# Performance work log

Measured on AMD Instinct MI355X. Metric: run time of the kernel, lower is better.

Reference implementation:

```python
import jax, jax.numpy as jnp
import numpy as np

N, D, T = 8192, 512, 262144
MARGIN = 1.0


def setup_inputs() -> dict:
    key = jax.random.key(0)
    k_emb, k_a, k_p, k_n = jax.random.split(key, 4)
    embeddings = jax.random.normal(k_emb, (N, D), dtype=jnp.float32)
    ind_anch = jax.random.randint(k_a, (T,), 0, N, dtype=jnp.int64 if jax.config.jax_enable_x64 else jnp.int32)
    ind_pos = jax.random.randint(k_p, (T,), 0, N, dtype=ind_anch.dtype)
    ind_neg = jax.random.randint(k_n, (T,), 0, N, dtype=ind_anch.dtype)
    return {"embeddings": embeddings, "ind_anch": ind_anch, "ind_pos": ind_pos, "ind_neg": ind_neg}


def reference(embeddings, ind_anch, ind_pos, ind_neg):
    # cosine distance matrix: 1 - normalized @ normalized.T  -> [N, N]
    emb_norm = embeddings / jnp.linalg.norm(embeddings, axis=1, keepdims=True)
    dist_matrix = 1.0 - jnp.matmul(emb_norm, emb_norm.T)
    dist_pos = dist_matrix[ind_anch, ind_pos]
    dist_neg = dist_matrix[ind_anch, ind_neg]
    loss = jax.nn.relu(dist_pos - dist_neg + MARGIN)
    return loss.mean()
```

## Files before the change

### kernel.cpp

```cpp
#include <hip/hip_runtime.h>

constexpr int N_EMB = 8192;
constexpr int D_EMB = 512;
constexpr int T_TRI = 262144;
#define MARGIN_F 1.0f

constexpr int GRID_TRIP = 8192;
constexpr float QSCALE = 512.0f;
constexpr float INV_QS2 = 1.0f / (QSCALE * QSCALE);

constexpr size_t TAB_BYTES = (size_t)N_EMB * D_EMB;

#if __has_builtin(__builtin_amdgcn_sdot4)
__device__ __forceinline__ int dot4(int a, int b, int c) {
    return __builtin_amdgcn_sdot4(a, b, c, false);
}
#else
__device__ __forceinline__ int dot4(int a, int b, int c) {
    c += ((int)(a << 24) >> 24) * ((int)(b << 24) >> 24);
    c += ((int)(a << 16) >> 24) * ((int)(b << 16) >> 24);
    c += ((int)(a <<  8) >> 24) * ((int)(b <<  8) >> 24);
    c += (a >> 24) * (b >> 24);
    return c;
}
#endif

__global__ __launch_bounds__(256) void prep_kernel(const float* __restrict__ emb,
                                                   unsigned char* __restrict__ tab) {
    const int lane = threadIdx.x & 63;
    const int row  = (blockIdx.x << 2) + (threadIdx.x >> 6);
    const float4* p = (const float4*)(emb + (size_t)row * D_EMB);
    float4 v0 = p[2 * lane];
    float4 v1 = p[2 * lane + 1];
    float s = v0.x * v0.x + v0.y * v0.y + v0.z * v0.z + v0.w * v0.w
            + v1.x * v1.x + v1.y * v1.y + v1.z * v1.z + v1.w * v1.w;
#pragma unroll
    for (int off = 32; off > 0; off >>= 1) s += __shfl_xor(s, off, 64);
    const float scl = rsqrtf(s) * QSCALE;

    float q[8] = {v0.x, v0.y, v0.z, v0.w, v1.x, v1.y, v1.z, v1.w};
    int qi[8];
#pragma unroll
    for (int i = 0; i < 8; ++i) {
        float f = rintf(q[i] * scl);
        f = fmaxf(-127.0f, fminf(127.0f, f));
        qi[i] = (int)f;
    }
    unsigned w0 = (qi[0] & 255) | ((qi[1] & 255) << 8) | ((qi[2] & 255) << 16) | ((unsigned)(qi[3] & 255) << 24);
    unsigned w1 = (qi[4] & 255) | ((qi[5] & 255) << 8) | ((qi[6] & 255) << 16) | ((unsigned)(qi[7] & 255) << 24);
    uint2 o; o.x = w0; o.y = w1;
    *(uint2*)(tab + (size_t)row * D_EMB + 8 * lane) = o;
}

__global__ __launch_bounds__(256) void triplet_kernel(const unsigned char* __restrict__ tab,
                                                      const int* __restrict__ ind_a,
                                                      const int* __restrict__ ind_p,
                                                      const int* __restrict__ ind_n,
                                                      float* __restrict__ part) {
    const int lane   = threadIdx.x & 63;
    const int waveIb = threadIdx.x >> 6;
    const int waveId = (blockIdx.x << 2) + waveIb;
    const int tbase  = waveId << 3;

    const int slot = lane & 7;
    const int arr  = lane >> 3;
    const int* ptr = (arr == 0) ? ind_a : ((arr == 1) ? ind_p : ind_n);
    const int myidx = ptr[tbase + slot];

    const int q   = lane >> 4;
    const int sub = lane & 15;
    const int boff = sub << 4;

    const int ia0 = __shfl(myidx, q, 64);
    const int ip0 = __shfl(myidx, 8 + q, 64);
    const int in0 = __shfl(myidx, 16 + q, 64);
    const int ia1 = __shfl(myidx, 4 + q, 64);
    const int ip1 = __shfl(myidx, 12 + q, 64);
    const int in1 = __shfl(myidx, 20 + q, 64);

    const unsigned char* pa0 = tab + ((size_t)ia0 << 9) + boff;
    const unsigned char* pp0 = tab + ((size_t)ip0 << 9) + boff;
    const unsigned char* pn0 = tab + ((size_t)in0 << 9) + boff;
    const unsigned char* pa1 = tab + ((size_t)ia1 << 9) + boff;
    const unsigned char* pp1 = tab + ((size_t)ip1 << 9) + boff;
    const unsigned char* pn1 = tab + ((size_t)in1 << 9) + boff;

    uint4 a00 = *(const uint4*)pa0,        a01 = *(const uint4*)(pa0 + 256);
    uint4 p00 = *(const uint4*)pp0,        p01 = *(const uint4*)(pp0 + 256);
    uint4 n00 = *(const uint4*)pn0,        n01 = *(const uint4*)(pn0 + 256);
    uint4 a10 = *(const uint4*)pa1,        a11 = *(const uint4*)(pa1 + 256);
    uint4 p10 = *(const uint4*)pp1,        p11 = *(const uint4*)(pp1 + 256);
    uint4 n10 = *(const uint4*)pn1,        n11 = *(const uint4*)(pn1 + 256);

    float local = 0.0f;

    {
        int sp = 0, sn = 0;
        sp = dot4((int)a00.x, (int)p00.x, sp); sp = dot4((int)a00.y, (int)p00.y, sp);
        sp = dot4((int)a00.z, (int)p00.z, sp); sp = dot4((int)a00.w, (int)p00.w, sp);
        sp = dot4((int)a01.x, (int)p01.x, sp); sp = dot4((int)a01.y, (int)p01.y, sp);
        sp = dot4((int)a01.z, (int)p01.z, sp); sp = dot4((int)a01.w, (int)p01.w, sp);
        sn = dot4((int)a00.x, (int)n00.x, sn); sn = dot4((int)a00.y, (int)n00.y, sn);
        sn = dot4((int)a00.z, (int)n00.z, sn); sn = dot4((int)a00.w, (int)n00.w, sn);
        sn = dot4((int)a01.x, (int)n01.x, sn); sn = dot4((int)a01.y, (int)n01.y, sn);
        sn = dot4((int)a01.z, (int)n01.z, sn); sn = dot4((int)a01.w, (int)n01.w, sn);
        int d = sn - sp;
#pragma unroll
        for (int m = 1; m < 16; m <<= 1) d += __shfl_xor(d, m, 64);
        if (sub == 0) local += fmaxf(fmaf((float)d, INV_QS2, MARGIN_F), 0.0f);
    }

    {
        int sp = 0, sn = 0;
        sp = dot4((int)a10.x, (int)p10.x, sp); sp = dot4((int)a10.y, (int)p10.y, sp);
        sp = dot4((int)a10.z, (int)p10.z, sp); sp = dot4((int)a10.w, (int)p10.w, sp);
        sp = dot4((int)a11.x, (int)p11.x, sp); sp = dot4((int)a11.y, (int)p11.y, sp);
        sp = dot4((int)a11.z, (int)p11.z, sp); sp = dot4((int)a11.w, (int)p11.w, sp);
        sn = dot4((int)a10.x, (int)n10.x, sn); sn = dot4((int)a10.y, (int)n10.y, sn);
        sn = dot4((int)a10.z, (int)n10.z, sn); sn = dot4((int)a10.w, (int)n10.w, sn);
        sn = dot4((int)a11.x, (int)n11.x, sn); sn = dot4((int)a11.y, (int)n11.y, sn);
        sn = dot4((int)a11.z, (int)n11.z, sn); sn = dot4((int)a11.w, (int)n11.w, sn);
        int d = sn - sp;
#pragma unroll
        for (int m = 1; m < 16; m <<= 1) d += __shfl_xor(d, m, 64);
        if (sub == 0) local += fmaxf(fmaf((float)d, INV_QS2, MARGIN_F), 0.0f);
    }

    local += __shfl_xor(local, 16, 64);
    local += __shfl_xor(local, 32, 64);

    __shared__ float smem[4];
    if (lane == 0) smem[waveIb] = local;
    __syncthreads();
    if (threadIdx.x == 0) {
        part[blockIdx.x] = smem[0] + smem[1] + smem[2] + smem[3];
    }
}

__global__ __launch_bounds__(256) void reduce_kernel(const float* __restrict__ part,
                                                     float* __restrict__ out) {
    float s = 0.0f;
#pragma unroll
    for (int i = 0; i < GRID_TRIP / 256; ++i) s += part[threadIdx.x + 256 * i];
#pragma unroll
    for (int off = 32; off > 0; off >>= 1) s += __shfl_down(s, off, 64);
    __shared__ float sm[4];
    if ((threadIdx.x & 63) == 0) sm[threadIdx.x >> 6] = s;
    __syncthreads();
    if (threadIdx.x == 0) {
        out[0] = (sm[0] + sm[1] + sm[2] + sm[3]) * (1.0f / (float)T_TRI);
    }
}

extern "C" void kernel_launch(void* const* d_in, const int* in_sizes, int n_in,
                              void* d_out, int out_size, void* d_ws, size_t ws_size,
                              hipStream_t stream) {
    const float* emb   = (const float*)d_in[0];
    const int*   ind_a = (const int*)d_in[1];
    const int*   ind_p = (const int*)d_in[2];
    const int*   ind_n = (const int*)d_in[3];
    float* out = (float*)d_out;

    unsigned char* tab = (unsigned char*)d_ws;
    float* part = (float*)((char*)d_ws + TAB_BYTES);

    prep_kernel<<<N_EMB / 4, 256, 0, stream>>>(emb, tab);
    triplet_kernel<<<GRID_TRIP, 256, 0, stream>>>(tab, ind_a, ind_p, ind_n, part);
    reduce_kernel<<<1, 256, 0, stream>>>(part, out);
}
```

Baseline: 92.15 us.

## Process 32 triplets per wave with register double-buffered row gathers

Each wave now handles 32 triplets instead of 8, and the grid shrinks from 8192 to 2048 blocks. Indices are loaded with coalesced per-array reads, and each iteration prefetches the next group's anchor, positive and negative rows into registers while the current group's dot products run. This amortises per-block launch and index overhead and keeps more gathers in flight per wave. The cost is higher register pressure and fewer waves available to hide latency, which the launch bound of 4 blocks is meant to contain.

After: 89.82 us. 2.5% less time.

```diff
diff --git a/kernel.cpp b/kernel.cpp
--- a/kernel.cpp
+++ b/kernel.cpp
@@ -5,7 +5,7 @@
 constexpr int T_TRI = 262144;
 #define MARGIN_F 1.0f
 
-constexpr int GRID_TRIP = 8192;
+constexpr int GRID_TRIP = 2048;
 constexpr float QSCALE = 512.0f;
 constexpr float INV_QS2 = 1.0f / (QSCALE * QSCALE);
 
@@ -52,78 +52,68 @@
     *(uint2*)(tab + (size_t)row * D_EMB + 8 * lane) = o;
 }
 
-__global__ __launch_bounds__(256) void triplet_kernel(const unsigned char* __restrict__ tab,
-                                                      const int* __restrict__ ind_a,
-                                                      const int* __restrict__ ind_p,
-                                                      const int* __restrict__ ind_n,
-                                                      float* __restrict__ part) {
+__global__ __launch_bounds__(256, 4) void triplet_kernel(const unsigned char* __restrict__ tab,
+                                                         const int* __restrict__ ind_a,
+                                                         const int* __restrict__ ind_p,
+                                                         const int* __restrict__ ind_n,
+                                                         float* __restrict__ part) {
     const int lane   = threadIdx.x & 63;
     const int waveIb = threadIdx.x >> 6;
     const int waveId = (blockIdx.x << 2) + waveIb;
-    const int tbase  = waveId << 3;
+    const int tbase  = waveId << 5;
 
-    const int slot = lane & 7;
-    const int arr  = lane >> 3;
-    const int* ptr = (arr == 0) ? ind_a : ((arr == 1) ? ind_p : ind_n);
-    const int myidx = ptr[tbase + slot];
+    const int l5 = lane & 31;
+    const int idxA = ind_a[tbase + l5];
+    const int idxP = ind_p[tbase + l5];
+    const int idxN = ind_n[tbase + l5];
 
-    const int q   = lane >> 4;
-    const int sub = lane & 15;
+    const int q    = lane >> 4;
+    const int sub  = lane & 15;
     const int boff = sub << 4;
 
-    const int ia0 = __shfl(myidx, q, 64);
-    const int ip0 = __shfl(myidx, 8 + q, 64);
-    const int in0 = __shfl(myidx, 16 + q, 64);
-    const int ia1 = __shfl(myidx, 4 + q, 64);
-    const int ip1 = __shfl(myidx, 12 + q, 64);
-    const int in1 = __shfl(myidx, 20 + q, 64);
-
-    const unsigned char* pa0 = tab + ((size_t)ia0 << 9) + boff;
-    const unsigned char* pp0 = tab + ((size_t)ip0 << 9) + boff;
-    const unsigned char* pn0 = tab + ((size_t)in0 << 9) + boff;
-    const unsigned char* pa1 = tab + ((size_t)ia1 << 9) + boff;
-    const unsigned char* pp1 = tab + ((size_t)ip1 << 9) + boff;
-    const unsigned char* pn1 = tab + ((size_t)in1 << 9) + boff;
-
-    uint4 a00 = *(const uint4*)pa0,        a01 = *(const uint4*)(pa0 + 256);
-    uint4 p00 = *(const uint4*)pp0,        p01 = *(const uint4*)(pp0 + 256);
-    uint4 n00 = *(const uint4*)pn0,        n01 = *(const uint4*)(pn0 + 256);
-    uint4 a10 = *(const uint4*)pa1,        a11 = *(const uint4*)(pa1 + 256);
-    uint4 p10 = *(const uint4*)pp1,        p11 = *(const uint4*)(pp1 + 256);
-    uint4 n10 = *(const uint4*)pn1,        n11 = *(const uint4*)(pn1 + 256);
+    int s0 = q;
+    int ia = __shfl(idxA, s0, 64);
+    int ip = __shfl(idxP, s0, 64);
+    int in_ = __shfl(idxN, s0, 64);
+    const uint4* pa = (const uint4*)(tab + ((size_t)ia << 9) + boff);
+    const uint4* pp = (const uint4*)(tab + ((size_t)ip << 9) + boff);
+    const uint4* pn = (const uint4*)(tab + ((size_t)in_ << 9) + boff);
+    uint4 a0 = pa[0], a1 = pa[16];
+    uint4 p0 = pp[0], p1 = pp[16];
+    uint4 n0 = pn[0], n1 = pn[16];
 
     float local = 0.0f;
+#pragma unroll
+    for (int g = 0; g < 8; ++g) {
+        uint4 ba0, ba1, bp0, bp1, bn0, bn1;
+        if (g < 7) {
+            const int s = 4 * (g + 1) + q;
+            const int ja = __shfl(idxA, s, 64);
+            const int jp = __shfl(idxP, s, 64);
+            const int jn = __shfl(idxN, s, 64);
+            const uint4* qa = (const uint4*)(tab + ((size_t)ja << 9) + boff);
+            const uint4* qp = (const uint4*)(tab + ((size_t)jp << 9) + boff);
+            const uint4* qn = (const uint4*)(tab + ((size_t)jn << 9) + boff);
+            ba0 = qa[0]; ba1 = qa[16];
+            bp0 = qp[0]; bp1 = qp[16];
+            bn0 = qn[0]; bn1 = qn[16];
+        }
 
-    {
         int sp = 0, sn = 0;
-        sp = dot4((int)a00.x, (int)p00.x, sp); sp = dot4((int)a00.y, (int)p00.y, sp);
-        sp = dot4((int)a00.z, (int)p00.z, sp); sp = dot4((int)a00.w, (int)p00.w, sp);
-        sp = dot4((int)a01.x, (int)p01.x, sp); sp = dot4((int)a01.y, (int)p01.y, sp);
-        sp = dot4((int)a01.z, (int)p01.z, sp); sp = dot4((int)a01.w, (int)p01.w, sp);
-        sn = dot4((int)a00.x, (int)n00.x, sn); sn = dot4((int)a00.y, (int)n00.y, sn);
-        sn = dot4((int)a00.z, (int)n00.z, sn); sn = dot4((int)a00.w, (int)n00.w, sn);
-        sn = dot4((int)a01.x, (int)n01.x, sn); sn = dot4((int)a01.y, (int)n01.y, sn);
-        sn = dot4((int)a01.z, (int)n01.z, sn); sn = dot4((int)a01.w, (int)n01.w, sn);
+        sp = dot4((int)a0.x, (int)p0.x, sp); sp = dot4((int)a0.y, (int)p0.y, sp);
+        sp = dot4((int)a0.z, (int)p0.z, sp); sp = dot4((int)a0.w, (int)p0.w, sp);
+        sp = dot4((int)a1.x, (int)p1.x, sp); sp = dot4((int)a1.y, (int)p1.y, sp);
+        sp = dot4((int)a1.z, (int)p1.z, sp); sp = dot4((int)a1.w, (int)p1.w, sp);
+        sn = dot4((int)a0.x, (int)n0.x, sn); sn = dot4((int)a0.y, (int)n0.y, sn);
+        sn = dot4((int)a0.z, (int)n0.z, sn); sn = dot4((int)a0.w, (int)n0.w, sn);
+        sn = dot4((int)a1.x, (int)n1.x, sn); sn = dot4((int)a1.y, (int)n1.y, sn);
+        sn = dot4((int)a1.z, (int)n1.z, sn); sn = dot4((int)a1.w, (int)n1.w, sn);
         int d = sn - sp;
 #pragma unroll
         for (int m = 1; m < 16; m <<= 1) d += __shfl_xor(d, m, 64);
         if (sub == 0) local += fmaxf(fmaf((float)d, INV_QS2, MARGIN_F), 0.0f);
-    }
 
-    {
-        int sp = 0, sn = 0;
-        sp = dot4((int)a10.x, (int)p10.x, sp); sp = dot4((int)a10.y, (int)p10.y, sp);
-        sp = dot4((int)a10.z, (int)p10.z, sp); sp = dot4((int)a10.w, (int)p10.w, sp);
-        sp = dot4((int)a11.x, (int)p11.x, sp); sp = dot4((int)a11.y, (int)p11.y, sp);
-        sp = dot4((int)a11.z, (int)p11.z, sp); sp = dot4((int)a11.w, (int)p11.w, sp);
-        sn = dot4((int)a10.x, (int)n10.x, sn); sn = dot4((int)a10.y, (int)n10.y, sn);
-        sn = dot4((int)a10.z, (int)n10.z, sn); sn = dot4((int)a10.w, (int)n10.w, sn);
-        sn = dot4((int)a11.x, (int)n11.x, sn); sn = dot4((int)a11.y, (int)n11.y, sn);
-        sn = dot4((int)a11.z, (int)n11.z, sn); sn = dot4((int)a11.w, (int)n11.w, sn);
-        int d = sn - sp;
-#pragma unroll
-        for (int m = 1; m < 16; m <<= 1) d += __shfl_xor(d, m, 64);
-        if (sub == 0) local += fmaxf(fmaf((float)d, INV_QS2, MARGIN_F), 0.0f);
+        a0 = ba0; a1 = ba1; p0 = bp0; p1 = bp1; n0 = bn0; n1 = bn1;
     }
 
     local += __shfl_xor(local, 16, 64);
```
